# Optimization experiments

Measured on AMD Instinct MI355X. Metric: run time of the kernel, lower is better.

The kernel has to match this reference:

```python
import jax, jax.numpy as jnp
import numpy as np

D_MODEL = 1024
NUM_HEADS = 16
HEAD_DIM = D_MODEL // NUM_HEADS


def setup_inputs() -> dict:
    key = jax.random.key(0)
    ks = jax.random.split(key, 11)
    B, S = 2, 2048
    scale = 1.0 / np.sqrt(D_MODEL)
    inp = {
        "query": jax.random.normal(ks[0], (B, S, D_MODEL), jnp.float32),
        "key": jax.random.normal(ks[1], (B, S, D_MODEL), jnp.float32),
        "value": jax.random.normal(ks[2], (B, S, D_MODEL), jnp.float32),
        "Wq": jax.random.normal(ks[3], (D_MODEL, D_MODEL), jnp.float32) * scale,
        "bq": jnp.zeros((D_MODEL,), jnp.float32),
        "Wk": jax.random.normal(ks[4], (D_MODEL, D_MODEL), jnp.float32) * scale,
        "bk": jnp.zeros((D_MODEL,), jnp.float32),
        "Wv": jax.random.normal(ks[5], (D_MODEL, D_MODEL), jnp.float32) * scale,
        "bv": jnp.zeros((D_MODEL,), jnp.float32),
        "Wo": jax.random.normal(ks[6], (D_MODEL, D_MODEL), jnp.float32) * scale,
        "bo": jnp.zeros((D_MODEL,), jnp.float32),
    }
    return inp


def _split_heads(x):
    # [B, S, D] -> [B, H, S, Dh]
    B, S, _ = x.shape
    return x.reshape(B, S, NUM_HEADS, HEAD_DIM).transpose(0, 2, 1, 3)


def reference(query, key, value, Wq, bq, Wk, bk, Wv, bv, Wo, bo):
    q = _split_heads(query @ Wq.T + bq)   # [B,H,S,Dh]
    k = _split_heads(key @ Wk.T + bk)
    v = _split_heads(value @ Wv.T + bv)
    scores = jnp.einsum('bhqd,bhkd->bhqk', q, k) / jnp.sqrt(
        jnp.asarray(HEAD_DIM, q.dtype))
    probs = jax.nn.softmax(scores, axis=-1)
    ctx = jnp.einsum('bhqk,bhkd->bhqd', probs, v)  # [B,H,S,Dh]
    B, H, S, Dh = ctx.shape
    ctx = ctx.transpose(0, 2, 1, 3).reshape(B, S, H * Dh)  # [B,S,D]
    return ctx @ Wo.T + bo
```

## Files before the change

### kernel.cpp

```cpp
#include <hip/hip_runtime.h>
#include <hip/hip_bf16.h>
#include <stdint.h>

#define D_MODEL 1024
#define NHEADS  16
#define HDIM    64
#define BATCH   2
#define SEQ     2048
#define MROWS   (BATCH*SEQ)

typedef __attribute__((ext_vector_type(8))) short  bf16x8;
typedef __attribute__((ext_vector_type(4))) float  f32x4;
typedef __attribute__((ext_vector_type(4))) int    int4v;

__device__ __forceinline__ unsigned short f2bf(float f) {
  unsigned int u = __float_as_uint(f);
  u = (u + 0x7fffu + ((u >> 16) & 1u)) >> 16;
  return (unsigned short)u;
}

__device__ __forceinline__ unsigned cvtpk_bf16(float lo, float hi) {
  unsigned r;
  asm("v_cvt_pk_bf16_f32 %0, %1, %2" : "=v"(r) : "v"(lo), "v"(hi));
  return r;
}

__device__ __forceinline__ int4v pack8(const float4& x, const float4& y) {
  int4v r;
  r[0] = (int)cvtpk_bf16(x.x, x.y);
  r[1] = (int)cvtpk_bf16(x.z, x.w);
  r[2] = (int)cvtpk_bf16(y.x, y.y);
  r[3] = (int)cvtpk_bf16(y.z, y.w);
  return r;
}

__device__ __forceinline__ void gload_lds16(const unsigned short* g, unsigned short* l) {
  __builtin_amdgcn_global_load_lds(
      (const __attribute__((address_space(1))) void*)g,
      (__attribute__((address_space(3))) void*)l,
      16, 0, 0);
}

__device__ __forceinline__ int swz_chunk(int row) { return (row + (row >> 3)) & 7; }
__device__ __forceinline__ int swz4(int row) { return (row + (row >> 2)) & 3; }
__device__ __forceinline__ int kperm(int m) {
  return (m & 0x63) | ((m & 0x10) >> 2) | ((m & 0x0C) << 1);
}

__global__ __launch_bounds__(256, 3) void gemm_qkv128(
    const float* __restrict__ Xq, const float* __restrict__ Xk,
    const float* __restrict__ Xv,
    const float* __restrict__ Wq, const float* __restrict__ Wk,
    const float* __restrict__ Wv,
    const float* __restrict__ bq, const float* __restrict__ bk,
    const float* __restrict__ bv,
    unsigned short* __restrict__ oq, unsigned short* __restrict__ ok,
    unsigned short* __restrict__ ov) {
  __shared__ __align__(16) unsigned short LDS[2 * 8192];

  const int tid  = threadIdx.x;
  const int lane = tid & 63;
  const int wv   = tid >> 6;
  const int wr   = wv >> 1;
  const int wc   = wv & 1;
  const int g    = lane >> 4;
  const int cl   = lane & 15;

  int fid = blockIdx.x;
  int sid = (fid & 7) * 96 + (fid >> 3);
  int mt = sid / 24, nz = sid % 24;
  int z  = nz >> 3;
  int n0 = (nz & 7) * 128;
  int m0 = mt * 128;

  const float* X    = (z == 0) ? Xq : (z == 1) ? Xk : Xv;
  const float* W    = (z == 0) ? Wq : (z == 1) ? Wk : Wv;
  const float* bias = (z == 0) ? bq : (z == 1) ? bk : bv;
  float scale = (z == 0) ? 0.18033688011112042f : 1.0f;

  const int sr  = tid >> 1;
  const int sh  = tid & 1;
  const int ssw = swz4(sr);
  const float* Xrow = X + (size_t)(m0 + sr) * D_MODEL + sh * 16;
  const float* Wrow = W + (size_t)(n0 + sr) * D_MODEL + sh * 16;
  const int wb0 = sr * 64 + (((2 * sh) ^ ssw) << 4);
  const int wb1 = sr * 64 + (((2 * sh + 1) ^ ssw) << 4);

  float4 rA[4], rB[4];
  auto load_t = [&](int t) {
    const float* pa = Xrow + t * 32;
    rA[0] = *(const float4*)(pa);     rA[1] = *(const float4*)(pa + 4);
    rA[2] = *(const float4*)(pa + 8); rA[3] = *(const float4*)(pa + 12);
    const float* pb = Wrow + t * 32;
    rB[0] = *(const float4*)(pb);     rB[1] = *(const float4*)(pb + 4);
    rB[2] = *(const float4*)(pb + 8); rB[3] = *(const float4*)(pb + 12);
  };
  auto write_t = [&](int bi) {
    char* A_ = (char*)(LDS + bi * 8192);
    char* B_ = A_ + 8192;
    *(int4v*)(A_ + wb0) = pack8(rA[0], rA[1]);
    *(int4v*)(A_ + wb1) = pack8(rA[2], rA[3]);
    *(int4v*)(B_ + wb0) = pack8(rB[0], rB[1]);
    *(int4v*)(B_ + wb1) = pack8(rB[2], rB[3]);
  };

  f32x4 acc[4][4] = {};

  load_t(0);
  write_t(0);
  __syncthreads();

  for (int t = 0; t < 32; ++t) {
    if (t < 31) load_t(t + 1);
    __builtin_amdgcn_sched_barrier(0);
    const char* Ab = (const char*)(LDS + (t & 1) * 8192);
    const char* Bb = Ab + 8192;
    bf16x8 af[4], bfr[4];
#pragma unroll
    for (int i = 0; i < 4; ++i) {
      int row = wr * 64 + i * 16 + cl;
      af[i] = *(const bf16x8*)(Ab + row * 64 + ((g ^ swz4(row)) << 4));
    }
#pragma unroll
    for (int j = 0; j < 4; ++j) {
      int row = wc * 64 + j * 16 + cl;
      bfr[j] = *(const bf16x8*)(Bb + row * 64 + ((g ^ swz4(row)) << 4));
    }
    __builtin_amdgcn_s_setprio(1);
#pragma unroll
    for (int i = 0; i < 4; ++i)
#pragma unroll
      for (int j = 0; j < 4; ++j)
        acc[i][j] = __builtin_amdgcn_mfma_f32_16x16x32_bf16(af[i], bfr[j],
                                                            acc[i][j], 0, 0, 0);
    __builtin_amdgcn_s_setprio(0);
    if (t < 31) write_t((t + 1) & 1);
    __syncthreads();
  }

  if (z == 2) {
    int b = m0 >> 11;
    int sbase = (m0 & 2047) + wr * 64 + g * 4;
#pragma unroll
    for (int nj = 0; nj < 4; ++nj) {
      int n = n0 + wc * 64 + nj * 16 + cl;
      float bn = bias[n];
      unsigned short* vrow = ov + ((size_t)(b * 1024 + n)) * 2048;
#pragma unroll
      for (int mi = 0; mi < 4; ++mi) {
        int s = sbase + mi * 16;
        uint2 val;
        val.x = cvtpk_bf16(acc[mi][nj][0] + bn, acc[mi][nj][1] + bn);
        val.y = cvtpk_bf16(acc[mi][nj][2] + bn, acc[mi][nj][3] + bn);
        *(uint2*)(vrow + s) = val;
      }
    }
  } else {
    unsigned short* outp = (z == 0) ? oq : ok;
#pragma unroll
    for (int mi = 0; mi < 4; ++mi)
#pragma unroll
      for (int nj = 0; nj < 4; ++nj) {
        int n = n0 + wc * 64 + nj * 16 + cl;
        float bn = bias[n];
        int h = n >> 6, dh = n & 63;
#pragma unroll
        for (int r = 0; r < 4; ++r) {
          int m = m0 + wr * 64 + mi * 16 + g * 4 + r;
          float val = (acc[mi][nj][r] + bn) * scale;
          int b = m >> 11, s = m & 2047;
          outp[(((size_t)(b * NHEADS + h)) * SEQ + s) * HDIM + dh] = f2bf(val);
        }
      }
  }
}

__global__ __launch_bounds__(512, 1) void gemm_out2(
    const unsigned short* __restrict__ Xc, const float* __restrict__ Wo,
    const float* __restrict__ bo, float* __restrict__ out) {
  __shared__ __align__(16) unsigned short LDS[2 * 8192];

  const int tid  = threadIdx.x;
  const int lane = tid & 63;
  const int w8   = tid >> 6;
  const int wr   = w8 >> 2;
  const int wc   = w8 & 3;
  const int g    = lane >> 4;
  const int cl   = lane & 15;

  int fid = blockIdx.x;
  int sid = (fid & 7) * 32 + (fid >> 3);
  int m0 = (sid >> 3) * 128;
  int n0 = (sid & 7) * 128;

  const int ar  = tid >> 2;
  const int as  = tid & 3;
  const int asw = swz4(ar);
  const unsigned short* Arow = Xc + (size_t)(m0 + ar) * D_MODEL + (as ^ asw) * 8;
  const float*          Brow = Wo + (size_t)(n0 + ar) * D_MODEL + (as ^ asw) * 8;
  const int bwb = ar * 64 + (as << 4);

  float4 rB0, rB1;
  auto gloadA = [&](int t, int bi) {
    gload_lds16(Arow + t * 32, LDS + bi * 8192 + tid * 8);
  };
  auto loadB = [&](int t) {
    const float* p = Brow + t * 32;
    rB0 = *(const float4*)(p);
    rB1 = *(const float4*)(p + 4);
  };
  auto writeB = [&](int bi) {
    char* B_ = (char*)(LDS + bi * 8192) + 8192;
    *(int4v*)(B_ + bwb) = pack8(rB0, rB1);
  };

  f32x4 acc[4][2] = {};

  gloadA(0, 0); loadB(0); writeB(0);
  __syncthreads();

#pragma unroll 2
  for (int t = 0; t < 32; ++t) {
    if (t < 31) { gloadA(t + 1, (t + 1) & 1); loadB(t + 1); }
    __builtin_amdgcn_sched_barrier(0);
    const char* Ab = (const char*)(LDS + (t & 1) * 8192);
    const char* Bb = Ab + 8192;
    bf16x8 af[4], bfr[2];
#pragma unroll
    for (int j = 0; j < 2; ++j) {
      int row = wc * 32 + j * 16 + cl;
      bfr[j] = *(const bf16x8*)(Bb + row * 64 + ((g ^ swz4(row)) << 4));
    }
#pragma unroll
    for (int i = 0; i < 4; ++i) {
      int row = wr * 64 + i * 16 + cl;
      af[i] = *(const bf16x8*)(Ab + row * 64 + ((g ^ swz4(row)) << 4));
    }
    __builtin_amdgcn_s_setprio(1);
#pragma unroll
    for (int i = 0; i < 4; ++i)
#pragma unroll
      for (int j = 0; j < 2; ++j)
        acc[i][j] = __builtin_amdgcn_mfma_f32_16x16x32_bf16(af[i], bfr[j],
                                                            acc[i][j], 0, 0, 0);
    __builtin_amdgcn_s_setprio(0);
    if (t < 31) writeB((t + 1) & 1);
    __syncthreads();
  }

#pragma unroll
  for (int mi = 0; mi < 4; ++mi)
#pragma unroll
    for (int nj = 0; nj < 2; ++nj) {
      int n = n0 + wc * 32 + nj * 16 + cl;
      float bn = bo[n];
#pragma unroll
      for (int r = 0; r < 4; ++r) {
        int m = m0 + wr * 64 + mi * 16 + g * 4 + r;
        out[(size_t)m * D_MODEL + n] = acc[mi][nj][r] + bn;
      }
    }
}

__global__ __launch_bounds__(256, 2) void attn(
    const unsigned short* __restrict__ q, const unsigned short* __restrict__ k,
    const unsigned short* __restrict__ vt, unsigned short* __restrict__ ctx) {
  __shared__ __align__(16) unsigned short K0[128 * 64], V0[64 * 128];
  __shared__ __align__(16) unsigned short K1[128 * 64], V1[64 * 128];

  const int tid  = threadIdx.x;
  const int lane = tid & 63;
  const int wv   = tid >> 6;
  const int g    = lane >> 4;
  const int cl   = lane & 15;

  const int bh = blockIdx.x;
  const int qt = blockIdx.y;

  const unsigned short* qb  = q  + (size_t)bh * SEQ * HDIM;
  const unsigned short* kb  = k  + (size_t)bh * SEQ * HDIM;
  const unsigned short* vbt = vt + (size_t)bh * HDIM * SEQ;

  bf16x8 qf[2][2];
  {
    int qbase = qt * 128 + wv * 32;
#pragma unroll
    for (int qh = 0; qh < 2; ++qh) {
      const unsigned short* qp = qb + (size_t)(qbase + qh * 16 + cl) * HDIM + 8 * g;
      qf[qh][0] = *(const bf16x8*)(qp);
      qf[qh][1] = *(const bf16x8*)(qp + 32);
    }
  }

  const int srowK = tid >> 3;
  const int swzK  = swz_chunk(srowK);
  const int vrow  = tid >> 4;
  const int swzV  = swz_chunk(vrow);
  const int ldst  = tid * 16;

  f32x4 acc0[4] = {}, acc1[4] = {};
  f32x4 accs0 = {}, accs1 = {};
  const int4v onesi = {0x3F803F80, 0x3F803F80, 0x3F803F80, 0x3F803F80};
  const bf16x8 onesb = __builtin_bit_cast(bf16x8, onesi);

  auto stageK_ = [&](int t, unsigned short* Kb) {
    const unsigned short* kt_ = kb + (size_t)t * 128 * HDIM;
#pragma unroll
    for (int c = 0; c < 4; ++c) {
      int row  = srowK + 32 * c;
      int col  = ((tid & 7) ^ swzK ^ ((c & 1) << 2)) * 8;
      gload_lds16(kt_ + (size_t)kperm(row) * HDIM + col,
                  (unsigned short*)((char*)Kb + ldst + c * 4096));
    }
  };
  auto stageV_ = [&](int t, unsigned short* Vb) {
    const unsigned short* vt_ = vbt + t * 128;
#pragma unroll
    for (int c = 0; c < 4; ++c) {
      int row = vrow + 16 * c;
      int sw  = (swzV + 2 * c) & 7;
      int col = (((tid & 7) ^ sw) | (tid & 8)) * 8;
      gload_lds16(vt_ + (size_t)row * SEQ + col,
                  (unsigned short*)((char*)Vb + ldst + c * 4096));
    }
  };

  f32x4 sc[8][2];

  auto qk = [&](const unsigned short* Kb) {
#pragma unroll
    for (int ni = 0; ni < 8; ++ni) { sc[ni][0] = f32x4{}; sc[ni][1] = f32x4{}; }
    __builtin_amdgcn_s_setprio(1);
#pragma unroll
    for (int kc = 0; kc < 2; ++kc)
#pragma unroll
      for (int ni = 0; ni < 8; ++ni) {
        int row  = ni * 16 + cl;
        int byte = row * 128 + (((kc * 4 + g) ^ swz_chunk(row)) << 4);
        bf16x8 kf = *(const bf16x8*)((const char*)Kb + byte);
        sc[ni][0] = __builtin_amdgcn_mfma_f32_16x16x32_bf16(kf, qf[0][kc], sc[ni][0], 0, 0, 0);
        sc[ni][1] = __builtin_amdgcn_mfma_f32_16x16x32_bf16(kf, qf[1][kc], sc[ni][1], 0, 0, 0);
      }
    __builtin_amdgcn_s_setprio(0);
  };

  auto smpack = [&](int4v (&pa0)[4], int4v (&pa1)[4]) {
#pragma unroll
    for (int qh = 0; qh < 2; ++qh)
#pragma unroll
      for (int ni = 0; ni < 8; ++ni)
#pragma unroll
        for (int r = 0; r < 4; ++r)
          sc[ni][qh][r] = __builtin_amdgcn_exp2f(sc[ni][qh][r]);
#pragma unroll
    for (int kcp = 0; kcp < 4; ++kcp) {
      pa0[kcp][0] = (int)cvtpk_bf16(sc[2 * kcp][0][0], sc[2 * kcp][0][1]);
      pa0[kcp][1] = (int)cvtpk_bf16(sc[2 * kcp][0][2], sc[2 * kcp][0][3]);
      pa0[kcp][2] = (int)cvtpk_bf16(sc[2 * kcp + 1][0][0], sc[2 * kcp + 1][0][1]);
      pa0[kcp][3] = (int)cvtpk_bf16(sc[2 * kcp + 1][0][2], sc[2 * kcp + 1][0][3]);
      pa1[kcp][0] = (int)cvtpk_bf16(sc[2 * kcp][1][0], sc[2 * kcp][1][1]);
      pa1[kcp][1] = (int)cvtpk_bf16(sc[2 * kcp][1][2], sc[2 * kcp][1][3]);
      pa1[kcp][2] = (int)cvtpk_bf16(sc[2 * kcp + 1][1][0], sc[2 * kcp + 1][1][1]);
      pa1[kcp][3] = (int)cvtpk_bf16(sc[2 * kcp + 1][1][2], sc[2 * kcp + 1][1][3]);
    }
  };

  auto pv = [&](const unsigned short* Vb, int4v (&pa0)[4], int4v (&pa1)[4]) {
    __builtin_amdgcn_s_setprio(1);
#pragma unroll
    for (int kcp = 0; kcp < 4; ++kcp) {
      bf16x8 a0 = __builtin_bit_cast(bf16x8, pa0[kcp]);
      bf16x8 a1 = __builtin_bit_cast(bf16x8, pa1[kcp]);
#pragma unroll
      for (int nd = 0; nd < 4; ++nd) {
        int row = nd * 16 + cl;
        int c   = kcp * 4 + g;
        int byte = row * 256 + ((((c & 7) ^ swz_chunk(row)) | (c & 8)) << 4);
        bf16x8 vf = *(const bf16x8*)((const char*)Vb + byte);
        acc0[nd] = __builtin_amdgcn_mfma_f32_16x16x32_bf16(a0, vf, acc0[nd], 0, 0, 0);
        acc1[nd] = __builtin_amdgcn_mfma_f32_16x16x32_bf16(a1, vf, acc1[nd], 0, 0, 0);
      }
      accs0 = __builtin_amdgcn_mfma_f32_16x16x32_bf16(a0, onesb, accs0, 0, 0, 0);
      accs1 = __builtin_amdgcn_mfma_f32_16x16x32_bf16(a1, onesb, accs1, 0, 0, 0);
    }
    __builtin_amdgcn_s_setprio(0);
  };

  const int NT = SEQ / 128;
  stageK_(0, K0);
  stageV_(0, V0);
  __syncthreads();
  stageK_(1, K1);
  qk(K0);
  for (int i = 0; i < NT; ++i) {
    int4v pa0[4], pa1[4];
    smpack(pa0, pa1);
    __syncthreads();
    if (i + 2 < NT) stageK_(i + 2, (i & 1) ? K1 : K0);
    if (i + 1 < NT) stageV_(i + 1, (i & 1) ? V0 : V1);
    if (i + 1 < NT) qk((i & 1) ? K0 : K1);
    pv((i & 1) ? V1 : V0, pa0, pa1);
  }

  int b = bh >> 4, h = bh & 15;
#pragma unroll
  for (int r = 0; r < 4; ++r) {
    float i0 = 1.0f / accs0[r];
    float i1 = 1.0f / accs1[r];
#pragma unroll
    for (int qh = 0; qh < 2; ++qh) {
      int srow_o = qt * 128 + wv * 32 + qh * 16 + g * 4 + r;
      float iv = qh ? i1 : i0;
#pragma unroll
      for (int nd = 0; nd < 4; ++nd) {
        int d = nd * 16 + cl;
        float val = (qh ? acc1[nd][r] : acc0[nd][r]) * iv;
        ctx[(((size_t)(b * SEQ + srow_o)) * NHEADS + h) * HDIM + d] = f2bf(val);
      }
    }
  }
}

extern "C" void kernel_launch(void* const* d_in, const int* in_sizes, int n_in,
                              void* d_out, int out_size, void* d_ws, size_t ws_size,
                              hipStream_t stream) {
  (void)in_sizes; (void)n_in; (void)out_size; (void)ws_size;
  const float* query = (const float*)d_in[0];
  const float* key_  = (const float*)d_in[1];
  const float* value = (const float*)d_in[2];
  const float* Wq = (const float*)d_in[3];
  const float* bq = (const float*)d_in[4];
  const float* Wk = (const float*)d_in[5];
  const float* bk = (const float*)d_in[6];
  const float* Wv = (const float*)d_in[7];
  const float* bv = (const float*)d_in[8];
  const float* Wo = (const float*)d_in[9];
  const float* bo = (const float*)d_in[10];
  float* out = (float*)d_out;

  unsigned short* w = (unsigned short*)d_ws;
  const size_t NA = (size_t)MROWS * D_MODEL;
  unsigned short* qs  = w;
  unsigned short* ks  = qs + NA;
  unsigned short* vtb = ks + NA;
  unsigned short* cx  = vtb + NA;

  gemm_qkv128<<<dim3(768, 1, 1), 256, 0, stream>>>(query, key_, value, Wq, Wk, Wv,
                                                   bq, bk, bv, qs, ks, vtb);
  attn<<<dim3(32, 16, 1), 256, 0, stream>>>(qs, ks, vtb, cx);
  gemm_out2<<<dim3(256, 1, 1), 512, 0, stream>>>(cx, Wo, bo, out);
}
```

Baseline: 130.2 us.

## Pre-convert QKV inputs and weights to bf16, use direct-to-LDS loads in GEMM

Adds a conversion kernel that writes bf16 copies of the query, key and value activations and the three projection weights into workspace. The QKV projection GEMM then stages bf16 tiles straight into LDS with global_load_lds and an XOR swizzle, replacing the register double-buffered fp32 load-and-pack path. This halves the bytes the GEMM re-reads per tile and removes in-loop conversion. In exchange it adds a full extra memory pass and launch, and the new GEMM loop is single-buffered with two barriers per k-step.

```diff
diff --git a/kernel.cpp b/kernel.cpp
--- a/kernel.cpp
+++ b/kernel.cpp
@@ -47,96 +47,108 @@
   return (m & 0x63) | ((m & 0x10) >> 2) | ((m & 0x0C) << 1);
 }
 
-__global__ __launch_bounds__(256, 3) void gemm_qkv128(
-    const float* __restrict__ Xq, const float* __restrict__ Xk,
-    const float* __restrict__ Xv,
-    const float* __restrict__ Wq, const float* __restrict__ Wk,
-    const float* __restrict__ Wv,
+struct CvtArgs {
+  const float* src[6];
+  unsigned short* dst[6];
+  int n[6];
+};
+
+__global__ __launch_bounds__(256) void cvt_all(CvtArgs a) {
+  int t = blockIdx.y;
+  const float* s = a.src[t];
+  unsigned short* d = a.dst[t];
+  int n = a.n[t];
+  int stride = gridDim.x * blockDim.x * 4;
+  for (int i = (blockIdx.x * blockDim.x + threadIdx.x) * 4; i < n; i += stride) {
+    float4 v = *(const float4*)(s + i);
+    ushort4 o;
+    o.x = f2bf(v.x); o.y = f2bf(v.y); o.z = f2bf(v.z); o.w = f2bf(v.w);
+    *(ushort4*)(d + i) = o;
+  }
+}
+
+__device__ __forceinline__ void gemm_core(const unsigned short* __restrict__ X,
+                                          const unsigned short* __restrict__ W,
+                                          int m0, int n0,
+                                          unsigned short* As, unsigned short* Bs,
+                                          f32x4 (&acc)[4][4]) {
+  const int tid  = threadIdx.x;
+  const int lane = tid & 63;
+  const int wv   = tid >> 6;
+  const int wr   = wv >> 1, wc = wv & 1;
+  const int srow = tid >> 3;
+  const int scol = (((tid & 7) ^ (srow & 7)) * 8);
+  const int sdst = tid * 16;
+
+  for (int kt = 0; kt < D_MODEL / 64; ++kt) {
+    __syncthreads();
+    const unsigned short* Xs = X + (size_t)m0 * D_MODEL + kt * 64;
+    const unsigned short* Ws = W + (size_t)n0 * D_MODEL + kt * 64;
+#pragma unroll
+    for (int c = 0; c < 4; ++c) {
+      gload_lds16(Xs + (size_t)(srow + c * 32) * D_MODEL + scol,
+                  (unsigned short*)((char*)As + sdst + c * 4096));
+      gload_lds16(Ws + (size_t)(srow + c * 32) * D_MODEL + scol,
+                  (unsigned short*)((char*)Bs + sdst + c * 4096));
+    }
+    __syncthreads();
+#pragma unroll
+    for (int kc = 0; kc < 2; ++kc) {
+      bf16x8 af[4], bfv[4];
+#pragma unroll
+      for (int i = 0; i < 4; ++i) {
+        int arow  = wr * 64 + i * 16 + (lane & 15);
+        int abyte = (arow * 128 + (kc * 32 + 8 * (lane >> 4)) * 2) ^ ((arow & 7) << 4);
+        af[i] = *(const bf16x8*)((const char*)As + abyte);
+        int brow  = wc * 64 + i * 16 + (lane & 15);
+        int bbyte = (brow * 128 + (kc * 32 + 8 * (lane >> 4)) * 2) ^ ((brow & 7) << 4);
+        bfv[i] = *(const bf16x8*)((const char*)Bs + bbyte);
+      }
+#pragma unroll
+      for (int mi = 0; mi < 4; ++mi)
+#pragma unroll
+        for (int ni = 0; ni < 4; ++ni)
+          acc[mi][ni] = __builtin_amdgcn_mfma_f32_16x16x32_bf16(af[mi], bfv[ni],
+                                                                acc[mi][ni], 0, 0, 0);
+    }
+  }
+}
+
+__global__ __launch_bounds__(256) void gemm_qkv(
+    const unsigned short* __restrict__ Xq, const unsigned short* __restrict__ Xk,
+    const unsigned short* __restrict__ Xv,
+    const unsigned short* __restrict__ Wq, const unsigned short* __restrict__ Wk,
+    const unsigned short* __restrict__ Wv,
     const float* __restrict__ bq, const float* __restrict__ bk,
     const float* __restrict__ bv,
     unsigned short* __restrict__ oq, unsigned short* __restrict__ ok,
     unsigned short* __restrict__ ov) {
-  __shared__ __align__(16) unsigned short LDS[2 * 8192];
-
-  const int tid  = threadIdx.x;
-  const int lane = tid & 63;
-  const int wv   = tid >> 6;
-  const int wr   = wv >> 1;
-  const int wc   = wv & 1;
+  __shared__ __align__(16) unsigned short As[128 * 64];
+  __shared__ __align__(16) unsigned short Bs[128 * 64];
+
+  int fid   = blockIdx.x;
+  int xcd   = fid & 7;
+  int r_    = fid >> 3;
+  int mloc  = r_ / 3;
+  int nzloc = r_ % 3;
+  int nz    = xcd * 3 + nzloc;
+  int z     = nz >> 3;
+  int n0    = (nz & 7) * 128;
+  int m0    = mloc * 128;
+
+  const unsigned short* X = (z == 0) ? Xq : (z == 1) ? Xk : Xv;
+  const unsigned short* W = (z == 0) ? Wq : (z == 1) ? Wk : Wv;
+  const float* bias       = (z == 0) ? bq : (z == 1) ? bk : bv;
+  float scale = (z == 0) ? 0.18033688011112042f : 1.0f;
+
+  f32x4 acc[4][4] = {};
+  gemm_core(X, W, m0, n0, As, Bs, acc);
+
+  const int lane = threadIdx.x & 63;
+  const int wv   = threadIdx.x >> 6;
+  const int wr   = wv >> 1, wc = wv & 1;
   const int g    = lane >> 4;
   const int cl   = lane & 15;
-
-  int fid = blockIdx.x;
-  int sid = (fid & 7) * 96 + (fid >> 3);
-  int mt = sid / 24, nz = sid % 24;
-  int z  = nz >> 3;
-  int n0 = (nz & 7) * 128;
-  int m0 = mt * 128;
-
-  const float* X    = (z == 0) ? Xq : (z == 1) ? Xk : Xv;
-  const float* W    = (z == 0) ? Wq : (z == 1) ? Wk : Wv;
-  const float* bias = (z == 0) ? bq : (z == 1) ? bk : bv;
-  float scale = (z == 0) ? 0.18033688011112042f : 1.0f;
-
-  const int sr  = tid >> 1;
-  const int sh  = tid & 1;
-  const int ssw = swz4(sr);
-  const float* Xrow = X + (size_t)(m0 + sr) * D_MODEL + sh * 16;
-  const float* Wrow = W + (size_t)(n0 + sr) * D_MODEL + sh * 16;
-  const int wb0 = sr * 64 + (((2 * sh) ^ ssw) << 4);
-  const int wb1 = sr * 64 + (((2 * sh + 1) ^ ssw) << 4);
-
-  float4 rA[4], rB[4];
-  auto load_t = [&](int t) {
-    const float* pa = Xrow + t * 32;
-    rA[0] = *(const float4*)(pa);     rA[1] = *(const float4*)(pa + 4);
-    rA[2] = *(const float4*)(pa + 8); rA[3] = *(const float4*)(pa + 12);
-    const float* pb = Wrow + t * 32;
-    rB[0] = *(const float4*)(pb);     rB[1] = *(const float4*)(pb + 4);
-    rB[2] = *(const float4*)(pb + 8); rB[3] = *(const float4*)(pb + 12);
-  };
-  auto write_t = [&](int bi) {
-    char* A_ = (char*)(LDS + bi * 8192);
-    char* B_ = A_ + 8192;
-    *(int4v*)(A_ + wb0) = pack8(rA[0], rA[1]);
-    *(int4v*)(A_ + wb1) = pack8(rA[2], rA[3]);
-    *(int4v*)(B_ + wb0) = pack8(rB[0], rB[1]);
-    *(int4v*)(B_ + wb1) = pack8(rB[2], rB[3]);
-  };
-
-  f32x4 acc[4][4] = {};
-
-  load_t(0);
-  write_t(0);
-  __syncthreads();
-
-  for (int t = 0; t < 32; ++t) {
-    if (t < 31) load_t(t + 1);
-    __builtin_amdgcn_sched_barrier(0);
-    const char* Ab = (const char*)(LDS + (t & 1) * 8192);
-    const char* Bb = Ab + 8192;
-    bf16x8 af[4], bfr[4];
-#pragma unroll
-    for (int i = 0; i < 4; ++i) {
-      int row = wr * 64 + i * 16 + cl;
-      af[i] = *(const bf16x8*)(Ab + row * 64 + ((g ^ swz4(row)) << 4));
-    }
-#pragma unroll
-    for (int j = 0; j < 4; ++j) {
-      int row = wc * 64 + j * 16 + cl;
-      bfr[j] = *(const bf16x8*)(Bb + row * 64 + ((g ^ swz4(row)) << 4));
-    }
-    __builtin_amdgcn_s_setprio(1);
-#pragma unroll
-    for (int i = 0; i < 4; ++i)
-#pragma unroll
-      for (int j = 0; j < 4; ++j)
-        acc[i][j] = __builtin_amdgcn_mfma_f32_16x16x32_bf16(af[i], bfr[j],
-                                                            acc[i][j], 0, 0, 0);
-    __builtin_amdgcn_s_setprio(0);
-    if (t < 31) write_t((t + 1) & 1);
-    __syncthreads();
-  }
 
   if (z == 2) {
     int b = m0 >> 11;
@@ -165,9 +177,9 @@
         float bn = bias[n];
         int h = n >> 6, dh = n & 63;
 #pragma unroll
-        for (int r = 0; r < 4; ++r) {
-          int m = m0 + wr * 64 + mi * 16 + g * 4 + r;
-          float val = (acc[mi][nj][r] + bn) * scale;
+        for (int rr = 0; rr < 4; ++rr) {
+          int m = m0 + wr * 64 + mi * 16 + g * 4 + rr;
+          float val = (acc[mi][nj][rr] + bn) * scale;
           int b = m >> 11, s = m & 2047;
           outp[(((size_t)(b * NHEADS + h)) * SEQ + s) * HDIM + dh] = f2bf(val);
         }
@@ -255,9 +267,9 @@
       int n = n0 + wc * 32 + nj * 16 + cl;
       float bn = bo[n];
 #pragma unroll
-      for (int r = 0; r < 4; ++r) {
-        int m = m0 + wr * 64 + mi * 16 + g * 4 + r;
-        out[(size_t)m * D_MODEL + n] = acc[mi][nj][r] + bn;
+      for (int rr = 0; rr < 4; ++rr) {
+        int m = m0 + wr * 64 + mi * 16 + g * 4 + rr;
+        out[(size_t)m * D_MODEL + n] = acc[mi][nj][rr] + bn;
       }
     }
 }
@@ -350,8 +362,8 @@
 #pragma unroll
       for (int ni = 0; ni < 8; ++ni)
 #pragma unroll
-        for (int r = 0; r < 4; ++r)
-          sc[ni][qh][r] = __builtin_amdgcn_exp2f(sc[ni][qh][r]);
+        for (int rr = 0; rr < 4; ++rr)
+          sc[ni][qh][rr] = __builtin_amdgcn_exp2f(sc[ni][qh][rr]);
 #pragma unroll
     for (int kcp = 0; kcp < 4; ++kcp) {
       pa0[kcp][0] = (int)cvtpk_bf16(sc[2 * kcp][0][0], sc[2 * kcp][0][1]);
@@ -404,17 +416,17 @@
 
   int b = bh >> 4, h = bh & 15;
 #pragma unroll
-  for (int r = 0; r < 4; ++r) {
-    float i0 = 1.0f / accs0[r];
-    float i1 = 1.0f / accs1[r];
+  for (int rr = 0; rr < 4; ++rr) {
+    float i0 = 1.0f / accs0[rr];
+    float i1 = 1.0f / accs1[rr];
 #pragma unroll
     for (int qh = 0; qh < 2; ++qh) {
-      int srow_o = qt * 128 + wv * 32 + qh * 16 + g * 4 + r;
+      int srow_o = qt * 128 + wv * 32 + qh * 16 + g * 4 + rr;
       float iv = qh ? i1 : i0;
 #pragma unroll
       for (int nd = 0; nd < 4; ++nd) {
         int d = nd * 16 + cl;
-        float val = (qh ? acc1[nd][r] : acc0[nd][r]) * iv;
+        float val = (qh ? acc1[nd][rr] : acc0[nd][rr]) * iv;
         ctx[(((size_t)(b * SEQ + srow_o)) * NHEADS + h) * HDIM + d] = f2bf(val);
       }
     }
@@ -440,13 +452,29 @@
 
   unsigned short* w = (unsigned short*)d_ws;
   const size_t NA = (size_t)MROWS * D_MODEL;
-  unsigned short* qs  = w;
+  const size_t NW = (size_t)D_MODEL * D_MODEL;
+  unsigned short* Xq  = w;
+  unsigned short* Xk  = Xq + NA;
+  unsigned short* Xv  = Xk + NA;
+  unsigned short* Wqb = Xv + NA;
+  unsigned short* Wkb = Wqb + NW;
+  unsigned short* Wvb = Wkb + NW;
+  unsigned short* qs  = Wvb + NW;
   unsigned short* ks  = qs + NA;
   unsigned short* vtb = ks + NA;
   unsigned short* cx  = vtb + NA;
 
-  gemm_qkv128<<<dim3(768, 1, 1), 256, 0, stream>>>(query, key_, value, Wq, Wk, Wv,
-                                                   bq, bk, bv, qs, ks, vtb);
+  CvtArgs ca;
+  ca.src[0] = query; ca.dst[0] = Xq;  ca.n[0] = (int)NA;
+  ca.src[1] = key_;  ca.dst[1] = Xk;  ca.n[1] = (int)NA;
+  ca.src[2] = value; ca.dst[2] = Xv;  ca.n[2] = (int)NA;
+  ca.src[3] = Wq;    ca.dst[3] = Wqb; ca.n[3] = (int)NW;
+  ca.src[4] = Wk;    ca.dst[4] = Wkb; ca.n[4] = (int)NW;
+  ca.src[5] = Wv;    ca.dst[5] = Wvb; ca.n[5] = (int)NW;
+
+  cvt_all<<<dim3(256, 6, 1), 256, 0, stream>>>(ca);
+  gemm_qkv<<<dim3(768, 1, 1), 256, 0, stream>>>(Xq, Xk, Xv, Wqb, Wkb, Wvb,
+                                                bq, bk, bv, qs, ks, vtb);
   attn<<<dim3(32, 16, 1), 256, 0, stream>>>(qs, ks, vtb, cx);
   gemm_out2<<<dim3(256, 1, 1), 512, 0, stream>>>(cx, Wo, bo, out);
 }
```

Result: faster. 126.9 us (-2.6%).

## Pre-convert QKV activations to bf16 and stream A tiles via direct LDS loads

Applied to the files above, without the earlier changes.

Adds a separate kernel that converts query/key/value from fp32 to bf16 in workspace. The QKV GEMM then loads its A tiles with global_load_lds straight into shared memory, skipping the register round-trip and in-kernel packing, while W is still converted on the fly. The block grows to 512 threads in a 2x4 wave layout, each wave owning a 64x32 sub-tile, and the tile-to-XCD mapping is changed. The extra launch and the write and reread of the bf16 activations (about 24MB read, 12MB written) may cost more than the conversion work it removes.

```diff
diff --git a/kernel.cpp b/kernel.cpp
--- a/kernel.cpp
+++ b/kernel.cpp
@@ -47,9 +47,29 @@
   return (m & 0x63) | ((m & 0x10) >> 2) | ((m & 0x0C) << 1);
 }
 
-__global__ __launch_bounds__(256, 3) void gemm_qkv128(
-    const float* __restrict__ Xq, const float* __restrict__ Xk,
-    const float* __restrict__ Xv,
+struct CvtArgs {
+  const float* src[3];
+  unsigned short* dst[3];
+  int n[3];
+};
+
+__global__ __launch_bounds__(256) void cvt_all(CvtArgs a) {
+  int t = blockIdx.y;
+  const float* s = a.src[t];
+  unsigned short* d = a.dst[t];
+  int n = a.n[t];
+  int stride = gridDim.x * blockDim.x * 4;
+  for (int i = (blockIdx.x * blockDim.x + threadIdx.x) * 4; i < n; i += stride) {
+    float4 v = *(const float4*)(s + i);
+    ushort4 o;
+    o.x = f2bf(v.x); o.y = f2bf(v.y); o.z = f2bf(v.z); o.w = f2bf(v.w);
+    *(ushort4*)(d + i) = o;
+  }
+}
+
+__global__ __launch_bounds__(512, 2) void gemm_qkv128(
+    const unsigned short* __restrict__ Xq, const unsigned short* __restrict__ Xk,
+    const unsigned short* __restrict__ Xv,
     const float* __restrict__ Wq, const float* __restrict__ Wk,
     const float* __restrict__ Wv,
     const float* __restrict__ bq, const float* __restrict__ bk,
@@ -60,81 +80,79 @@
 
   const int tid  = threadIdx.x;
   const int lane = tid & 63;
-  const int wv   = tid >> 6;
-  const int wr   = wv >> 1;
-  const int wc   = wv & 1;
+  const int w8   = tid >> 6;
+  const int wr   = w8 >> 2;
+  const int wc   = w8 & 3;
   const int g    = lane >> 4;
   const int cl   = lane & 15;
 
-  int fid = blockIdx.x;
-  int sid = (fid & 7) * 96 + (fid >> 3);
-  int mt = sid / 24, nz = sid % 24;
-  int z  = nz >> 3;
-  int n0 = (nz & 7) * 128;
-  int m0 = mt * 128;
-
-  const float* X    = (z == 0) ? Xq : (z == 1) ? Xk : Xv;
-  const float* W    = (z == 0) ? Wq : (z == 1) ? Wk : Wv;
-  const float* bias = (z == 0) ? bq : (z == 1) ? bk : bv;
+  int fid   = blockIdx.x;
+  int xcd   = fid & 7;
+  int r_    = fid >> 3;
+  int mloc  = r_ / 3;
+  int nzloc = r_ % 3;
+  int nz    = xcd * 3 + nzloc;
+  int z     = nz >> 3;
+  int n0    = (nz & 7) * 128;
+  int m0    = mloc * 128;
+
+  const unsigned short* X = (z == 0) ? Xq : (z == 1) ? Xk : Xv;
+  const float* W          = (z == 0) ? Wq : (z == 1) ? Wk : Wv;
+  const float* bias       = (z == 0) ? bq : (z == 1) ? bk : bv;
   float scale = (z == 0) ? 0.18033688011112042f : 1.0f;
 
-  const int sr  = tid >> 1;
-  const int sh  = tid & 1;
-  const int ssw = swz4(sr);
-  const float* Xrow = X + (size_t)(m0 + sr) * D_MODEL + sh * 16;
-  const float* Wrow = W + (size_t)(n0 + sr) * D_MODEL + sh * 16;
-  const int wb0 = sr * 64 + (((2 * sh) ^ ssw) << 4);
-  const int wb1 = sr * 64 + (((2 * sh + 1) ^ ssw) << 4);
-
-  float4 rA[4], rB[4];
-  auto load_t = [&](int t) {
-    const float* pa = Xrow + t * 32;
-    rA[0] = *(const float4*)(pa);     rA[1] = *(const float4*)(pa + 4);
-    rA[2] = *(const float4*)(pa + 8); rA[3] = *(const float4*)(pa + 12);
-    const float* pb = Wrow + t * 32;
-    rB[0] = *(const float4*)(pb);     rB[1] = *(const float4*)(pb + 4);
-    rB[2] = *(const float4*)(pb + 8); rB[3] = *(const float4*)(pb + 12);
-  };
-  auto write_t = [&](int bi) {
-    char* A_ = (char*)(LDS + bi * 8192);
-    char* B_ = A_ + 8192;
-    *(int4v*)(A_ + wb0) = pack8(rA[0], rA[1]);
-    *(int4v*)(A_ + wb1) = pack8(rA[2], rA[3]);
-    *(int4v*)(B_ + wb0) = pack8(rB[0], rB[1]);
-    *(int4v*)(B_ + wb1) = pack8(rB[2], rB[3]);
-  };
-
-  f32x4 acc[4][4] = {};
-
-  load_t(0);
-  write_t(0);
+  const int ar  = tid >> 2;
+  const int as  = tid & 3;
+  const int asw = swz4(ar);
+  const unsigned short* Arow = X + (size_t)(m0 + ar) * D_MODEL + (as ^ asw) * 8;
+  const float*          Brow = W + (size_t)(n0 + ar) * D_MODEL + (as ^ asw) * 8;
+  const int bwb = ar * 64 + (as << 4);
+
+  float4 rB0, rB1;
+  auto gloadA = [&](int t, int bi) {
+    gload_lds16(Arow + t * 32, LDS + bi * 8192 + tid * 8);
+  };
+  auto loadB = [&](int t) {
+    const float* p = Brow + t * 32;
+    rB0 = *(const float4*)(p);
+    rB1 = *(const float4*)(p + 4);
+  };
+  auto writeB = [&](int bi) {
+    char* B_ = (char*)(LDS + bi * 8192) + 8192;
+    *(int4v*)(B_ + bwb) = pack8(rB0, rB1);
+  };
+
+  f32x4 acc[4][2] = {};
+
+  gloadA(0, 0); loadB(0); writeB(0);
   __syncthreads();
 
+#pragma unroll 2
   for (int t = 0; t < 32; ++t) {
-    if (t < 31) load_t(t + 1);
+    if (t < 31) { gloadA(t + 1, (t + 1) & 1); loadB(t + 1); }
     __builtin_amdgcn_sched_barrier(0);
     const char* Ab = (const char*)(LDS + (t & 1) * 8192);
     const char* Bb = Ab + 8192;
-    bf16x8 af[4], bfr[4];
+    bf16x8 af[4], bfr[2];
+#pragma unroll
+    for (int j = 0; j < 2; ++j) {
+      int row = wc * 32 + j * 16 + cl;
+      bfr[j] = *(const bf16x8*)(Bb + row * 64 + ((g ^ swz4(row)) << 4));
+    }
 #pragma unroll
     for (int i = 0; i < 4; ++i) {
       int row = wr * 64 + i * 16 + cl;
       af[i] = *(const bf16x8*)(Ab + row * 64 + ((g ^ swz4(row)) << 4));
     }
-#pragma unroll
-    for (int j = 0; j < 4; ++j) {
-      int row = wc * 64 + j * 16 + cl;
-      bfr[j] = *(const bf16x8*)(Bb + row * 64 + ((g ^ swz4(row)) << 4));
-    }
     __builtin_amdgcn_s_setprio(1);
 #pragma unroll
     for (int i = 0; i < 4; ++i)
 #pragma unroll
-      for (int j = 0; j < 4; ++j)
+      for (int j = 0; j < 2; ++j)
         acc[i][j] = __builtin_amdgcn_mfma_f32_16x16x32_bf16(af[i], bfr[j],
                                                             acc[i][j], 0, 0, 0);
     __builtin_amdgcn_s_setprio(0);
-    if (t < 31) write_t((t + 1) & 1);
+    if (t < 31) writeB((t + 1) & 1);
     __syncthreads();
   }
 
@@ -142,8 +160,8 @@
     int b = m0 >> 11;
     int sbase = (m0 & 2047) + wr * 64 + g * 4;
 #pragma unroll
-    for (int nj = 0; nj < 4; ++nj) {
-      int n = n0 + wc * 64 + nj * 16 + cl;
+    for (int nj = 0; nj < 2; ++nj) {
+      int n = n0 + wc * 32 + nj * 16 + cl;
       float bn = bias[n];
       unsigned short* vrow = ov + ((size_t)(b * 1024 + n)) * 2048;
 #pragma unroll
@@ -160,8 +178,8 @@
 #pragma unroll
     for (int mi = 0; mi < 4; ++mi)
 #pragma unroll
-      for (int nj = 0; nj < 4; ++nj) {
-        int n = n0 + wc * 64 + nj * 16 + cl;
+      for (int nj = 0; nj < 2; ++nj) {
+        int n = n0 + wc * 32 + nj * 16 + cl;
         float bn = bias[n];
         int h = n >> 6, dh = n & 63;
 #pragma unroll
@@ -440,12 +458,21 @@
 
   unsigned short* w = (unsigned short*)d_ws;
   const size_t NA = (size_t)MROWS * D_MODEL;
-  unsigned short* qs  = w;
+  unsigned short* Xq  = w;
+  unsigned short* Xk  = Xq + NA;
+  unsigned short* Xv  = Xk + NA;
+  unsigned short* qs  = Xv + NA;
   unsigned short* ks  = qs + NA;
   unsigned short* vtb = ks + NA;
   unsigned short* cx  = vtb + NA;
 
-  gemm_qkv128<<<dim3(768, 1, 1), 256, 0, stream>>>(query, key_, value, Wq, Wk, Wv,
+  CvtArgs ca;
+  ca.src[0] = query; ca.dst[0] = Xq;  ca.n[0] = (int)NA;
+  ca.src[1] = key_;  ca.dst[1] = Xk;  ca.n[1] = (int)NA;
+  ca.src[2] = value; ca.dst[2] = Xv;  ca.n[2] = (int)NA;
+
+  cvt_all<<<dim3(256, 3, 1), 256, 0, stream>>>(ca);
+  gemm_qkv128<<<dim3(768, 1, 1), 512, 0, stream>>>(Xq, Xk, Xv, Wq, Wk, Wv,
                                                    bq, bk, bv, qs, ks, vtb);
   attn<<<dim3(32, 16, 1), 256, 0, stream>>>(qs, ks, vtb, cx);
   gemm_out2<<<dim3(256, 1, 1), 512, 0, stream>>>(cx, Wo, bo, out);
```

Measured after the change: 128.8 us. Within noise of the previous version (-1.1%).
